# Optimization experiments

Measured on AMD Instinct MI355X. Metric: run time of the kernel, lower is better.

## Reference

```python
import jax, jax.numpy as jnp
import numpy as np

B, S, H, HKV, D, BS = 2, 2048, 32, 8, 128, 16
HIDDEN = H * D            # 4096
G = H // HKV              # 4 query heads per kv head
NB = S // BS              # 128 blocks per sequence
SCALE = D ** -0.5


def setup_inputs() -> dict:
    key = jax.random.key(0)
    k1, k2, k3 = jax.random.split(key, 3)
    T = B * S
    hidden_states = jax.random.normal(k1, (T, HIDDEN), dtype=jnp.float32)
    w_qkv = jax.random.normal(k2, (HIDDEN, HIDDEN + 2 * HKV * D), dtype=jnp.float32) * 0.02
    w_out = jax.random.normal(k3, (HIDDEN, HIDDEN), dtype=jnp.float32) * 0.02
    k_cache = jnp.zeros((B * NB, HKV, BS, D), dtype=jnp.float32)
    v_cache = jnp.zeros((B * NB, HKV, BS, D), dtype=jnp.float32)
    block_tables = jnp.arange(B * NB, dtype=jnp.int32).reshape(B, NB)
    return {"hidden_states": hidden_states, "w_qkv": w_qkv, "w_out": w_out,
            "k_cache": k_cache, "v_cache": v_cache, "block_tables": block_tables}


def reference(hidden_states, w_qkv, w_out, k_cache, v_cache, block_tables):
    # qkv projection on packed tokens [T, hidden]
    qkv = hidden_states @ w_qkv
    q, k, v = jnp.split(qkv, [HIDDEN, HIDDEN + HKV * D], axis=-1)
    q = q.reshape(B, S, H, D)
    k = k.reshape(B, S, HKV, D)
    v = v.reshape(B, S, HKV, D)

    # --- paged KV store: scatter per-block pages into cache via block_tables ---
    # [B, NB, BS, HKV, D] -> page layout [B, NB, HKV, BS, D]
    k_pages = k.reshape(B, NB, BS, HKV, D).transpose(0, 1, 3, 2, 4)
    v_pages = v.reshape(B, NB, BS, HKV, D).transpose(0, 1, 3, 2, 4)
    k_cache = k_cache.at[block_tables].set(k_pages)
    v_cache = v_cache.at[block_tables].set(v_pages)

    # --- paged KV gather for prefill attention ---
    kg = k_cache[block_tables].transpose(0, 2, 1, 3, 4).reshape(B, HKV, S, D)
    vg = v_cache[block_tables].transpose(0, 2, 1, 3, 4).reshape(B, HKV, S, D)

    # GQA causal attention: group query heads per kv head
    qh = q.transpose(0, 2, 1, 3).reshape(B, HKV, G, S, D)
    scores = jnp.einsum('bhgqd,bhkd->bhgqk', qh, kg) * SCALE
    causal = jnp.tril(jnp.ones((S, S), dtype=bool))
    scores = jnp.where(causal, scores, -jnp.inf)
    attn = jax.nn.softmax(scores, axis=-1)
    out = jnp.einsum('bhgqk,bhkd->bhgqd', attn, vg)   # [B,HKV,G,S,D]
    out = out.reshape(B, H, S, D).transpose(0, 2, 1, 3).reshape(B * S, HIDDEN)
    return out @ w_out
```

## Files before the change

kernel.cpp:

```cpp
#include <hip/hip_runtime.h>

#define BB 2
#define SS 2048
#define HH 32
#define HKV 8
#define DD 128
#define HIDDEN 4096
#define NQK 6144
#define TT 4096
#define SCALE 0.08838834764831843f
#define SCALE_LOG2E 0.12751743444f

typedef __attribute__((ext_vector_type(8), __may_alias__)) short short8;
typedef __attribute__((ext_vector_type(4), __may_alias__)) short short4v;
typedef __attribute__((ext_vector_type(4), __may_alias__)) float floatx4;
typedef __attribute__((ext_vector_type(4), __may_alias__)) float f4;

__device__ __forceinline__ short f2bf(float x) {
    unsigned u = __builtin_bit_cast(unsigned, x);
    u += 0x7FFFu + ((u >> 16) & 1u);
    return (short)(u >> 16);
}

__device__ __forceinline__ void gload_lds16(const short* g, short* l) {
    __builtin_amdgcn_global_load_lds((const __attribute__((address_space(1))) void*)g,
                                     (__attribute__((address_space(3))) void*)l, 16, 0, 0);
}

__global__ __launch_bounds__(256) void prep_fused(const float* __restrict__ hs,
                                                  short* __restrict__ hsb,
                                                  const float* __restrict__ wq,
                                                  short* __restrict__ wqT,
                                                  const float* __restrict__ wo,
                                                  short* __restrict__ woT) {
    __shared__ float t[64][65];
    int bid = blockIdx.x, tid = threadIdx.x;
    if (bid < 16384) {
        int i = bid * 256 + tid;
        f4 v = ((const f4*)hs)[i];
        short4v o = { f2bf(v.x), f2bf(v.y), f2bf(v.z), f2bf(v.w) };
        ((short4v*)hsb)[i] = o;
        return;
    }
    bid -= 16384;
    const float* src; short* dst; int cols;
    if (bid < 6144) { src = wq; dst = wqT; cols = NQK; }
    else            { bid -= 6144; src = wo; dst = woT; cols = HIDDEN; }
    const int rows = HIDDEN;
    int ntx = cols >> 6;
    int c0 = (bid % ntx) * 64, r0 = (bid / ntx) * 64;
    int tx = tid & 15, ty = tid >> 4;
#pragma unroll
    for (int i = 0; i < 64; i += 16) {
        f4 v = *(const f4*)(src + (size_t)(r0 + ty + i) * cols + c0 + tx * 4);
        t[ty + i][tx * 4 + 0] = v.x;
        t[ty + i][tx * 4 + 1] = v.y;
        t[ty + i][tx * 4 + 2] = v.z;
        t[ty + i][tx * 4 + 3] = v.w;
    }
    __syncthreads();
    int ox = tid & 7, oy = tid >> 3;
#pragma unroll
    for (int i = 0; i < 64; i += 32) {
        int cc = oy + i;
        short8 s;
#pragma unroll
        for (int j = 0; j < 8; j++) s[j] = f2bf(t[ox * 8 + j][cc]);
        *(short8*)(dst + (size_t)(c0 + cc) * rows + r0 + ox * 8) = s;
    }
}

__global__ __launch_bounds__(256) void build_vt(const short* __restrict__ qkv,
                                                short* __restrict__ vt) {
    __shared__ short t[32][33];
    int tx = threadIdx.x, ty = threadIdx.y;
    int s0 = blockIdx.x * 32, d0 = blockIdx.y * 32;
    int bh = blockIdx.z; int b = bh >> 3, hk = bh & 7;
#pragma unroll
    for (int i = 0; i < 32; i += 8)
        t[ty + i][tx] = qkv[(size_t)(b * SS + s0 + ty + i) * NQK + 5120 + hk * DD + d0 + tx];
    __syncthreads();
#pragma unroll
    for (int i = 0; i < 32; i += 8)
        vt[(size_t)(bh * DD + d0 + ty + i) * SS + s0 + tx] = t[tx][ty + i];
}

template <int OUT_BF16, int NFRAG>
__global__ __launch_bounds__(512, 2) void gemm_bt(const short* __restrict__ A,
                                                  const short* __restrict__ Bt,
                                                  void* __restrict__ Cout,
                                                  int M, int N, int K) {
    (void)M;
    constexpr int BUFSZ = 16384 + NFRAG * 4096;
    __shared__ __align__(16) short smem[2 * BUFSZ];
    const int tid  = threadIdx.x;
    const int wave = tid >> 6, lane = tid & 63;
    const int qn = lane & 15, quad = lane >> 4;
    const int wm = wave >> 2, wn = wave & 3;

    int bid = blockIdx.y * gridDim.x + blockIdx.x;
    int xcd = bid & 7, idx = bid >> 3;
    int bnx = gridDim.x >> 2;
    int xm = xcd & 1, xn = xcd >> 1;
    int im = idx & 7, in_ = idx >> 3;
    const int m0 = (xm * 8 + im) * 256;
    const int n0 = (xn * bnx + in_) * (NFRAG * 64);

    const int NT = K >> 6;

    const int srow = tid >> 3;
    const int scg  = (tid & 7) ^ (srow & 7);
    const short* aS = A  + (size_t)(m0 + srow) * K + scg * 8;
    const short* bS = Bt + (size_t)(n0 + srow) * K + scg * 8;
    const int lwo = wave * 512;

#define STAGE_A(buf, blk, tt) gload_lds16(aS + (size_t)(blk) * 64 * K + (size_t)(tt) * 64, \
                                          smem + (buf) + (blk) * 4096 + lwo)
#define STAGE_B(buf, blk, tt) gload_lds16(bS + (size_t)(blk) * 64 * K + (size_t)(tt) * 64, \
                                          smem + (buf) + 16384 + (blk) * 4096 + lwo)
#define VMCNT_STEADY() do { if constexpr (NFRAG == 3) asm volatile("s_waitcnt vmcnt(7)" ::: "memory"); \
                            else                      asm volatile("s_waitcnt vmcnt(8)" ::: "memory"); } while (0)

    const int xorm  = (qn & 7) << 3;
    const int a_row = (wm * 128 + qn) * 64;
    const int b_row = (wn * (NFRAG * 16) + qn) * 64;
    const int col0  = (quad * 8) ^ xorm;
    const int col1  = col0 ^ 32;

#pragma unroll
    for (int blk = 0; blk < 4; blk++) STAGE_A(0, blk, 0);
#pragma unroll
    for (int blk = 0; blk < NFRAG; blk++) STAGE_B(0, blk, 0);
    if (NT > 1) {
#pragma unroll
        for (int blk = 0; blk < 4; blk++) STAGE_A(BUFSZ, blk, 1);
#pragma unroll
        for (int blk = 0; blk < NFRAG; blk++) STAGE_B(BUFSZ, blk, 1);
        VMCNT_STEADY();
    } else {
        asm volatile("s_waitcnt vmcnt(0)" ::: "memory");
    }
    __builtin_amdgcn_s_barrier();

    floatx4 acc[8][NFRAG] = {};

#pragma unroll 2
    for (int t = 0; t < NT; ++t) {
        const int cb = (t & 1) * BUFSZ;
        const short* Ab = smem + cb;
        const short* Bb = smem + cb + 16384;
        short8 a[4][2], b0[2][2], b1[NFRAG - 2][2], a2[4][2];

#pragma unroll
        for (int mt = 0; mt < 4; mt++) {
            a[mt][0] = *(const short8*)(Ab + a_row + mt * 1024 + col0);
            a[mt][1] = *(const short8*)(Ab + a_row + mt * 1024 + col1);
        }
#pragma unroll
        for (int nt = 0; nt < 2; nt++) {
            b0[nt][0] = *(const short8*)(Bb + b_row + nt * 1024 + col0);
            b0[nt][1] = *(const short8*)(Bb + b_row + nt * 1024 + col1);
        }
        asm volatile("s_waitcnt lgkmcnt(8)" ::: "memory");
        __builtin_amdgcn_s_barrier();
        asm volatile("s_waitcnt lgkmcnt(0)" ::: "memory");
        __builtin_amdgcn_s_setprio(1);
#pragma unroll
        for (int mt = 0; mt < 4; mt++)
#pragma unroll
            for (int nt = 0; nt < 2; nt++) {
                acc[mt][nt] = __builtin_amdgcn_mfma_f32_16x16x32_bf16(a[mt][0], b0[nt][0], acc[mt][nt], 0, 0, 0);
                acc[mt][nt] = __builtin_amdgcn_mfma_f32_16x16x32_bf16(a[mt][1], b0[nt][1], acc[mt][nt], 0, 0, 0);
            }
        __builtin_amdgcn_s_setprio(0);
        __builtin_amdgcn_s_barrier();

#pragma unroll
        for (int nb = 0; nb < NFRAG - 2; nb++) {
            b1[nb][0] = *(const short8*)(Bb + b_row + (2 + nb) * 1024 + col0);
            b1[nb][1] = *(const short8*)(Bb + b_row + (2 + nb) * 1024 + col1);
        }
        if (t + 2 < NT) { STAGE_A(cb, 0, t + 2); STAGE_A(cb, 2, t + 2); }
        __builtin_amdgcn_s_barrier();
        asm volatile("s_waitcnt lgkmcnt(0)" ::: "memory");
        __builtin_amdgcn_s_setprio(1);
#pragma unroll
        for (int mt = 0; mt < 4; mt++)
#pragma unroll
            for (int nb = 0; nb < NFRAG - 2; nb++) {
                acc[mt][2 + nb] = __builtin_amdgcn_mfma_f32_16x16x32_bf16(a[mt][0], b1[nb][0], acc[mt][2 + nb], 0, 0, 0);
                acc[mt][2 + nb] = __builtin_amdgcn_mfma_f32_16x16x32_bf16(a[mt][1], b1[nb][1], acc[mt][2 + nb], 0, 0, 0);
            }
        __builtin_amdgcn_s_setprio(0);
        __builtin_amdgcn_s_barrier();

#pragma unroll
        for (int mt = 0; mt < 4; mt++) {
            a2[mt][0] = *(const short8*)(Ab + 4096 + a_row + mt * 1024 + col0);
            a2[mt][1] = *(const short8*)(Ab + 4096 + a_row + mt * 1024 + col1);
        }
        if (t + 2 < NT) {
#pragma unroll
            for (int blk = 0; blk < NFRAG; blk++) STAGE_B(cb, blk, t + 2);
        }
        __builtin_amdgcn_s_barrier();
        asm volatile("s_waitcnt lgkmcnt(0)" ::: "memory");
        __builtin_amdgcn_s_setprio(1);
#pragma unroll
        for (int mt = 0; mt < 4; mt++)
#pragma unroll
            for (int nb = 0; nb < NFRAG - 2; nb++) {
                acc[4 + mt][2 + nb] = __builtin_amdgcn_mfma_f32_16x16x32_bf16(a2[mt][0], b1[nb][0], acc[4 + mt][2 + nb], 0, 0, 0);
                acc[4 + mt][2 + nb] = __builtin_amdgcn_mfma_f32_16x16x32_bf16(a2[mt][1], b1[nb][1], acc[4 + mt][2 + nb], 0, 0, 0);
            }
        __builtin_amdgcn_s_setprio(0);
        __builtin_amdgcn_s_barrier();

        if (t + 2 < NT) { STAGE_A(cb, 1, t + 2); STAGE_A(cb, 3, t + 2); }
        __builtin_amdgcn_s_setprio(1);
#pragma unroll
        for (int mt = 0; mt < 4; mt++)
#pragma unroll
            for (int nt = 0; nt < 2; nt++) {
                acc[4 + mt][nt] = __builtin_amdgcn_mfma_f32_16x16x32_bf16(a2[mt][0], b0[nt][0], acc[4 + mt][nt], 0, 0, 0);
                acc[4 + mt][nt] = __builtin_amdgcn_mfma_f32_16x16x32_bf16(a2[mt][1], b0[nt][1], acc[4 + mt][nt], 0, 0, 0);
            }
        __builtin_amdgcn_s_setprio(0);
        if (t + 2 < NT) VMCNT_STEADY();
        else            asm volatile("s_waitcnt vmcnt(0)" ::: "memory");
        __builtin_amdgcn_s_barrier();
    }
#undef STAGE_A
#undef STAGE_B
#undef VMCNT_STEADY

    const int erow = m0 + wm * 128 + quad * 4;
    const int ecol = n0 + wn * (NFRAG * 16) + qn;
#pragma unroll
    for (int mt = 0; mt < 8; mt++)
#pragma unroll
        for (int nt = 0; nt < NFRAG; nt++)
#pragma unroll
            for (int r = 0; r < 4; r++) {
                size_t off = (size_t)(erow + mt * 16 + r) * N + ecol + nt * 16;
                if (OUT_BF16) ((short*)Cout)[off] = f2bf(acc[mt][nt][r]);
                else          ((float*)Cout)[off] = acc[mt][nt][r];
            }
}

__global__ __launch_bounds__(512, 4) void attn_kernel(const short* __restrict__ qkv,
                                                      const short* __restrict__ vt,
                                                      short* __restrict__ out) {
    __shared__ __align__(16) short Kb[2 * 32 * 128];
    __shared__ __align__(16) short Vb[2 * 128 * 32];
    __shared__ __align__(16) short Ps[8 * 16 * 40];
    int tid = threadIdx.x, wave = tid >> 6, lane = tid & 63;
    int qn = lane & 15, quad = lane >> 4;
    int bid = blockIdx.x;
    int qt = 63 - (bid >> 4);
    int b  = (bid >> 3) & 1;
    int hk = bid & 7;
    int qb = qt * 32;
    int qh = wave >> 2;
    int h  = hk * 4 + (wave & 3);
    int bh = b * 8 + hk;
    int rowq = qb + qh * 16 + qn;

    short8 qf[4];
    {
        const short* qrow = qkv + (size_t)(b * SS + rowq) * NQK + h * DD;
#pragma unroll
        for (int c = 0; c < 4; c++) qf[c] = *(const short8*)(qrow + c * 32 + quad * 8);
    }
    const short8 onesv = { 0x3F80, 0x3F80, 0x3F80, 0x3F80, 0x3F80, 0x3F80, 0x3F80, 0x3F80 };
    floatx4 oacc[8] = {};
    floatx4 lacc = {};
    const int ntiles = qt + 1;

    const int kRow = tid >> 4;
    const int kCgp = (tid & 15) ^ (kRow & 7);
    const int vRow = tid >> 2;
    const int vCgp = (tid & 3) ^ ((vRow >> 1) & 3);
    const short* kSrc = qkv + (size_t)(b * SS) * NQK + HIDDEN + hk * DD + kCgp * 8;
    const short* vSrc = vt + (size_t)(bh * DD) * SS + vCgp * 8;
    short* kDst = Kb + wave * 512;
    short* vDst = Vb + wave * 512;

#define STAGEKV(buf, kb) do {                                                   \
        gload_lds16(kSrc + (size_t)((kb) + kRow) * NQK, kDst + (buf) * 4096);   \
        gload_lds16(vSrc + (size_t)vRow * SS + (kb),    vDst + (buf) * 4096);   \
    } while (0)

    STAGEKV(0, 0);
    __syncthreads();

    short* pw = Ps + wave * (16 * 40);
    for (int it = 0; it < ntiles; ++it) {
        const int kb = it * 32;
        const int cur = it & 1;
        if (it + 1 < ntiles) STAGEKV(cur ^ 1, kb + 32);
        const short* Kc = Kb + cur * 4096;
        const short* Vc = Vb + cur * 4096;

        floatx4 sc[2] = {};
#pragma unroll
        for (int c = 0; c < 4; c++) {
            int cg = (((c * 4 + quad) ^ (qn & 7)) * 8);
            short8 k0 = *(const short8*)(Kc + qn * 128 + cg);
            short8 k1 = *(const short8*)(Kc + (16 + qn) * 128 + cg);
            sc[0] = __builtin_amdgcn_mfma_f32_16x16x32_bf16(k0, qf[c], sc[0], 0, 0, 0);
            sc[1] = __builtin_amdgcn_mfma_f32_16x16x32_bf16(k1, qf[c], sc[1], 0, 0, 0);
        }

        const bool needMask = (kb + 31 > qb + qh * 16);
#pragma unroll
        for (int kt = 0; kt < 2; kt++) {
            float e[4];
#pragma unroll
            for (int r = 0; r < 4; r++) {
                float v = exp2f(sc[kt][r] * SCALE_LOG2E);
                bool masked = needMask && (kb + kt * 16 + quad * 4 + r > rowq);
                e[r] = masked ? 0.f : v;
            }
            short4v pk = { f2bf(e[0]), f2bf(e[1]), f2bf(e[2]), f2bf(e[3]) };
            *(short4v*)(pw + qn * 40 + kt * 16 + quad * 4) = pk;
        }
        short8 pf = *(const short8*)(pw + qn * 40 + quad * 8);

        __builtin_amdgcn_s_setprio(1);
#pragma unroll
        for (int dt = 0; dt < 8; dt++) {
            int vg = ((quad ^ ((qn >> 1) & 3)) * 8);
            short8 vf = *(const short8*)(Vc + (dt * 16 + qn) * 32 + vg);
            oacc[dt] = __builtin_amdgcn_mfma_f32_16x16x32_bf16(vf, pf, oacc[dt], 0, 0, 0);
        }
        lacc = __builtin_amdgcn_mfma_f32_16x16x32_bf16(onesv, pf, lacc, 0, 0, 0);
        __builtin_amdgcn_s_setprio(0);
        __syncthreads();
    }
#undef STAGEKV

    float inv = 1.0f / lacc[0];
    short* orow = out + (size_t)(b * SS + rowq) * HIDDEN + h * DD;
#pragma unroll
    for (int dt = 0; dt < 8; dt++) {
        short4v ov = { f2bf(oacc[dt][0] * inv), f2bf(oacc[dt][1] * inv),
                       f2bf(oacc[dt][2] * inv), f2bf(oacc[dt][3] * inv) };
        *(short4v*)(orow + dt * 16 + quad * 4) = ov;
    }
}

extern "C" void kernel_launch(void* const* d_in, const int* in_sizes, int n_in,
                              void* d_out, int out_size, void* d_ws, size_t ws_size,
                              hipStream_t stream) {
    (void)in_sizes; (void)n_in; (void)out_size; (void)ws_size;
    const float* hs    = (const float*)d_in[0];
    const float* w_qkv = (const float*)d_in[1];
    const float* w_out = (const float*)d_in[2];

    char* ws = (char*)d_ws;
    short* hsb   = (short*)(ws);
    short* wqkvT = (short*)(ws + 33554432);
    short* woutT = (short*)(ws + 83886080);
    short* qkv   = (short*)(ws + 117440512);
    short* vtb   = (short*)(ws + 167772160);
    short* attnb = (short*)(ws + 176160768);

    prep_fused<<<26624, 256, 0, stream>>>(hs, hsb, w_qkv, wqkvT, w_out, woutT);
    gemm_bt<1, 3><<<dim3(NQK / 192, TT / 256), 512, 0, stream>>>(hsb, wqkvT, qkv, TT, NQK, HIDDEN);
    build_vt<<<dim3(64, 4, 16), dim3(32, 8), 0, stream>>>(qkv, vtb);
    attn_kernel<<<1024, 512, 0, stream>>>(qkv, vtb, attnb);
    gemm_bt<0, 4><<<dim3(HIDDEN / 256, TT / 256), 512, 0, stream>>>(attnb, woutT, d_out, TT, HIDDEN, HIDDEN);
}
```

Baseline: 678.8 us.

## Software-pipeline LDS fragment loads across GEMM iterations to overlap with MFMA

Restructures the GEMM main loop so the first A/B fragments for the next K-tile are read from LDS at the end of the current iteration. LDS reads for later fragments are issued before the MFMA blocks that don't depend on them, with partial lgkmcnt waits. Global-to-LDS staging is moved to different phases, and the per-iteration barrier count drops from five to four. This aims to hide LDS latency behind MFMA work, at the cost of more live registers and tighter ordering constraints on buffer reuse.

```diff
diff --git a/kernel.cpp b/kernel.cpp
--- a/kernel.cpp
+++ b/kernel.cpp
@@ -120,6 +120,8 @@
                                           smem + (buf) + 16384 + (blk) * 4096 + lwo)
 #define VMCNT_STEADY() do { if constexpr (NFRAG == 3) asm volatile("s_waitcnt vmcnt(7)" ::: "memory"); \
                             else                      asm volatile("s_waitcnt vmcnt(8)" ::: "memory"); } while (0)
+#define LGKM_P1() do { if constexpr (NFRAG == 3) asm volatile("s_waitcnt lgkmcnt(2)" ::: "memory"); \
+                       else                      asm volatile("s_waitcnt lgkmcnt(4)" ::: "memory"); } while (0)
 
     const int xorm  = (qn & 7) << 3;
     const int a_row = (wm * 128 + qn) * 64;
@@ -143,96 +145,108 @@
     __builtin_amdgcn_s_barrier();
 
     floatx4 acc[8][NFRAG] = {};
+    short8 alo[4][2], ahi[4][2], b0[2][2], b1[NFRAG - 2][2];
+
+#pragma unroll
+    for (int mt = 0; mt < 4; mt++) {
+        alo[mt][0] = *(const short8*)(smem + a_row + mt * 1024 + col0);
+        alo[mt][1] = *(const short8*)(smem + a_row + mt * 1024 + col1);
+    }
+#pragma unroll
+    for (int nt = 0; nt < 2; nt++) {
+        b0[nt][0] = *(const short8*)(smem + 16384 + b_row + nt * 1024 + col0);
+        b0[nt][1] = *(const short8*)(smem + 16384 + b_row + nt * 1024 + col1);
+    }
 
 #pragma unroll 2
     for (int t = 0; t < NT; ++t) {
         const int cb = (t & 1) * BUFSZ;
         const short* Ab = smem + cb;
         const short* Bb = smem + cb + 16384;
-        short8 a[4][2], b0[2][2], b1[NFRAG - 2][2], a2[4][2];
-
-#pragma unroll
-        for (int mt = 0; mt < 4; mt++) {
-            a[mt][0] = *(const short8*)(Ab + a_row + mt * 1024 + col0);
-            a[mt][1] = *(const short8*)(Ab + a_row + mt * 1024 + col1);
-        }
-#pragma unroll
-        for (int nt = 0; nt < 2; nt++) {
-            b0[nt][0] = *(const short8*)(Bb + b_row + nt * 1024 + col0);
-            b0[nt][1] = *(const short8*)(Bb + b_row + nt * 1024 + col1);
-        }
-        asm volatile("s_waitcnt lgkmcnt(8)" ::: "memory");
-        __builtin_amdgcn_s_barrier();
-        asm volatile("s_waitcnt lgkmcnt(0)" ::: "memory");
-        __builtin_amdgcn_s_setprio(1);
-#pragma unroll
-        for (int mt = 0; mt < 4; mt++)
-#pragma unroll
-            for (int nt = 0; nt < 2; nt++) {
-                acc[mt][nt] = __builtin_amdgcn_mfma_f32_16x16x32_bf16(a[mt][0], b0[nt][0], acc[mt][nt], 0, 0, 0);
-                acc[mt][nt] = __builtin_amdgcn_mfma_f32_16x16x32_bf16(a[mt][1], b0[nt][1], acc[mt][nt], 0, 0, 0);
-            }
-        __builtin_amdgcn_s_setprio(0);
-        __builtin_amdgcn_s_barrier();
 
 #pragma unroll
         for (int nb = 0; nb < NFRAG - 2; nb++) {
             b1[nb][0] = *(const short8*)(Bb + b_row + (2 + nb) * 1024 + col0);
             b1[nb][1] = *(const short8*)(Bb + b_row + (2 + nb) * 1024 + col1);
         }
+        LGKM_P1();
+        __builtin_amdgcn_s_barrier();
         if (t + 2 < NT) { STAGE_A(cb, 0, t + 2); STAGE_A(cb, 2, t + 2); }
+        __builtin_amdgcn_s_setprio(1);
+#pragma unroll
+        for (int mt = 0; mt < 4; mt++)
+#pragma unroll
+            for (int nt = 0; nt < 2; nt++) {
+                acc[mt][nt] = __builtin_amdgcn_mfma_f32_16x16x32_bf16(alo[mt][0], b0[nt][0], acc[mt][nt], 0, 0, 0);
+                acc[mt][nt] = __builtin_amdgcn_mfma_f32_16x16x32_bf16(alo[mt][1], b0[nt][1], acc[mt][nt], 0, 0, 0);
+            }
+        __builtin_amdgcn_s_setprio(0);
+
+#pragma unroll
+        for (int mt = 0; mt < 4; mt++) {
+            ahi[mt][0] = *(const short8*)(Ab + 4096 + a_row + mt * 1024 + col0);
+            ahi[mt][1] = *(const short8*)(Ab + 4096 + a_row + mt * 1024 + col1);
+        }
+        asm volatile("s_waitcnt lgkmcnt(8)" ::: "memory");
         __builtin_amdgcn_s_barrier();
+        if (t + 2 < NT) {
+#pragma unroll
+            for (int blk = 0; blk < NFRAG; blk++) STAGE_B(cb, blk, t + 2);
+        }
+        __builtin_amdgcn_s_setprio(1);
+#pragma unroll
+        for (int mt = 0; mt < 4; mt++)
+#pragma unroll
+            for (int nb = 0; nb < NFRAG - 2; nb++) {
+                acc[mt][2 + nb] = __builtin_amdgcn_mfma_f32_16x16x32_bf16(alo[mt][0], b1[nb][0], acc[mt][2 + nb], 0, 0, 0);
+                acc[mt][2 + nb] = __builtin_amdgcn_mfma_f32_16x16x32_bf16(alo[mt][1], b1[nb][1], acc[mt][2 + nb], 0, 0, 0);
+            }
+        __builtin_amdgcn_s_setprio(0);
+
         asm volatile("s_waitcnt lgkmcnt(0)" ::: "memory");
+        __builtin_amdgcn_s_barrier();
+        if (t + 2 < NT) { STAGE_A(cb, 1, t + 2); STAGE_A(cb, 3, t + 2); }
         __builtin_amdgcn_s_setprio(1);
 #pragma unroll
         for (int mt = 0; mt < 4; mt++)
 #pragma unroll
             for (int nb = 0; nb < NFRAG - 2; nb++) {
-                acc[mt][2 + nb] = __builtin_amdgcn_mfma_f32_16x16x32_bf16(a[mt][0], b1[nb][0], acc[mt][2 + nb], 0, 0, 0);
-                acc[mt][2 + nb] = __builtin_amdgcn_mfma_f32_16x16x32_bf16(a[mt][1], b1[nb][1], acc[mt][2 + nb], 0, 0, 0);
-            }
-        __builtin_amdgcn_s_setprio(0);
-        __builtin_amdgcn_s_barrier();
-
-#pragma unroll
-        for (int mt = 0; mt < 4; mt++) {
-            a2[mt][0] = *(const short8*)(Ab + 4096 + a_row + mt * 1024 + col0);
-            a2[mt][1] = *(const short8*)(Ab + 4096 + a_row + mt * 1024 + col1);
-        }
-        if (t + 2 < NT) {
-#pragma unroll
-            for (int blk = 0; blk < NFRAG; blk++) STAGE_B(cb, blk, t + 2);
-        }
-        __builtin_amdgcn_s_barrier();
-        asm volatile("s_waitcnt lgkmcnt(0)" ::: "memory");
+                acc[4 + mt][2 + nb] = __builtin_amdgcn_mfma_f32_16x16x32_bf16(ahi[mt][0], b1[nb][0], acc[4 + mt][2 + nb], 0, 0, 0);
+                acc[4 + mt][2 + nb] = __builtin_amdgcn_mfma_f32_16x16x32_bf16(ahi[mt][1], b1[nb][1], acc[4 + mt][2 + nb], 0, 0, 0);
+            }
+        __builtin_amdgcn_s_setprio(0);
+
         __builtin_amdgcn_s_setprio(1);
 #pragma unroll
         for (int mt = 0; mt < 4; mt++)
 #pragma unroll
-            for (int nb = 0; nb < NFRAG - 2; nb++) {
-                acc[4 + mt][2 + nb] = __builtin_amdgcn_mfma_f32_16x16x32_bf16(a2[mt][0], b1[nb][0], acc[4 + mt][2 + nb], 0, 0, 0);
-                acc[4 + mt][2 + nb] = __builtin_amdgcn_mfma_f32_16x16x32_bf16(a2[mt][1], b1[nb][1], acc[4 + mt][2 + nb], 0, 0, 0);
-            }
-        __builtin_amdgcn_s_setprio(0);
-        __builtin_amdgcn_s_barrier();
-
-        if (t + 2 < NT) { STAGE_A(cb, 1, t + 2); STAGE_A(cb, 3, t + 2); }
-        __builtin_amdgcn_s_setprio(1);
-#pragma unroll
-        for (int mt = 0; mt < 4; mt++)
-#pragma unroll
             for (int nt = 0; nt < 2; nt++) {
-                acc[4 + mt][nt] = __builtin_amdgcn_mfma_f32_16x16x32_bf16(a2[mt][0], b0[nt][0], acc[4 + mt][nt], 0, 0, 0);
-                acc[4 + mt][nt] = __builtin_amdgcn_mfma_f32_16x16x32_bf16(a2[mt][1], b0[nt][1], acc[4 + mt][nt], 0, 0, 0);
-            }
-        __builtin_amdgcn_s_setprio(0);
-        if (t + 2 < NT) VMCNT_STEADY();
-        else            asm volatile("s_waitcnt vmcnt(0)" ::: "memory");
-        __builtin_amdgcn_s_barrier();
+                acc[4 + mt][nt] = __builtin_amdgcn_mfma_f32_16x16x32_bf16(ahi[mt][0], b0[nt][0], acc[4 + mt][nt], 0, 0, 0);
+                acc[4 + mt][nt] = __builtin_amdgcn_mfma_f32_16x16x32_bf16(ahi[mt][1], b0[nt][1], acc[4 + mt][nt], 0, 0, 0);
+            }
+        __builtin_amdgcn_s_setprio(0);
+        if (t + 1 < NT) {
+            if (t + 2 < NT) VMCNT_STEADY();
+            else            asm volatile("s_waitcnt vmcnt(0)" ::: "memory");
+            __builtin_amdgcn_s_barrier();
+            const short* Abn = smem + ((t + 1) & 1) * BUFSZ;
+            const short* Bbn = Abn + 16384;
+#pragma unroll
+            for (int mt = 0; mt < 4; mt++) {
+                alo[mt][0] = *(const short8*)(Abn + a_row + mt * 1024 + col0);
+                alo[mt][1] = *(const short8*)(Abn + a_row + mt * 1024 + col1);
+            }
+#pragma unroll
+            for (int nt = 0; nt < 2; nt++) {
+                b0[nt][0] = *(const short8*)(Bbn + b_row + nt * 1024 + col0);
+                b0[nt][1] = *(const short8*)(Bbn + b_row + nt * 1024 + col1);
+            }
+        }
     }
 #undef STAGE_A
 #undef STAGE_B
 #undef VMCNT_STEADY
+#undef LGKM_P1
 
     const int erow = m0 + wm * 128 + quad * 4;
     const int ecol = n0 + wn * (NFRAG * 16) + qn;
```

Result: no change. 672.1 us (-1.0%).
